# Kernel optimization log

Measured on AMD Instinct MI355X. Metric: run time of the kernel, lower is better.

The kernel has to match this reference:

```python
import jax, jax.numpy as jnp
import numpy as np

DIM = 1024
NUM_HEADS = 16
HEAD_DIM = DIM // NUM_HEADS
SCALE = float(np.sqrt(HEAD_DIM))
NEG = -1e9


def setup_inputs() -> dict:
    key = jax.random.key(0)
    ks = jax.random.split(key, 12)
    B, S = 2, 2048
    std = 1.0 / np.sqrt(DIM)
    inp = {
        'query': jax.random.normal(ks[0], (B, S, DIM), jnp.float32),
        'key': jax.random.normal(ks[1], (B, S, DIM), jnp.float32),
        'value': jax.random.normal(ks[2], (B, S, DIM), jnp.float32),
        'key_padding_mask': jnp.ones((B, S), jnp.int32),
        'Wq': jax.random.normal(ks[3], (DIM, DIM), jnp.float32) * std,
        'bq': jax.random.normal(ks[4], (DIM,), jnp.float32) * std,
        'Wk': jax.random.normal(ks[5], (DIM, DIM), jnp.float32) * std,
        'bk': jax.random.normal(ks[6], (DIM,), jnp.float32) * std,
        'Wv': jax.random.normal(ks[7], (DIM, DIM), jnp.float32) * std,
        'bv': jax.random.normal(ks[8], (DIM,), jnp.float32) * std,
        'Wo': jax.random.normal(ks[9], (DIM, DIM), jnp.float32) * std,
        'bo': jax.random.normal(ks[10], (DIM,), jnp.float32) * std,
    }
    return inp


def reference(query, key, value, key_padding_mask, Wq, bq, Wk, bk, Wv, bv, Wo, bo):
    B, S, _ = query.shape
    # QKV projections (torch Linear: x @ W.T + b), split heads -> [B,H,S,D]
    def proj(x, W, b):
        return (x @ W.T + b).reshape(B, -1, NUM_HEADS, HEAD_DIM).transpose(0, 2, 1, 3)
    Q = proj(query, Wq, bq)
    K = proj(key, Wk, bk)
    V = proj(value, Wv, bv)
    # scaled dot-product scores [B,H,Sq,Sk]
    scores = jnp.einsum('bhqd,bhkd->bhqk', Q, K) / SCALE
    # key padding mask: positions where mask == 0 are filled with -1e9
    pad = (key_padding_mask == 0)[:, None, None, :]  # [B,1,1,Sk]
    scores = jnp.where(pad, NEG, scores)
    attention_weights = jax.nn.softmax(scores, axis=-1)
    context = jnp.einsum('bhqk,bhkd->bhqd', attention_weights, V)
    context = context.transpose(0, 2, 1, 3).reshape(B, -1, DIM)
    out = context @ Wo.T + bo
    return out, attention_weights
```

## Files before the change

### kernel.cpp

```cpp
#include <hip/hip_runtime.h>
#include <hip/hip_bf16.h>
#include <stdint.h>

#define DIMM 1024
#define HEADS 16
#define HD 64
#define BB 2
#define SS 2048
#define NTOK (BB*SS)

typedef __attribute__((ext_vector_type(8))) __bf16 bf16x8;
typedef __attribute__((ext_vector_type(4))) __bf16 bf16x4;
typedef __attribute__((ext_vector_type(4))) float f32x4;

__device__ __forceinline__ f32x4 mfma16(bf16x8 a, bf16x8 b, f32x4 c) {
  return __builtin_amdgcn_mfma_f32_16x16x32_bf16(a, b, c, 0, 0, 0);
}

__device__ __forceinline__ void gload_lds16(const void* g, void* l) {
  __builtin_amdgcn_global_load_lds(
      (__attribute__((address_space(1))) void*)(void*)g,
      (__attribute__((address_space(3))) void*)l,
      16, 0, 0);
}

#define LOG2E 1.4426950408889634f
#define C2 (0.125f * LOG2E)
#define NBRAW (-8e9f)

struct CvtArgs {
  const float* src[7];
  __bf16* dst[7];
  int n[7];
};

__global__ __launch_bounds__(256) void cvt_kernel(CvtArgs a) {
  const int t = blockIdx.y;
  const long i = ((long)blockIdx.x * 256 + threadIdx.x) * 8;
  if (i >= a.n[t]) return;
  const float* s = a.src[t] + i;
  f32x4 x0 = *(const f32x4*)s;
  f32x4 x1 = *(const f32x4*)(s + 4);
  bf16x8 o;
  o[0] = (__bf16)x0[0]; o[1] = (__bf16)x0[1]; o[2] = (__bf16)x0[2]; o[3] = (__bf16)x0[3];
  o[4] = (__bf16)x1[0]; o[5] = (__bf16)x1[1]; o[6] = (__bf16)x1[2]; o[7] = (__bf16)x1[3];
  *(bf16x8*)(a.dst[t] + i) = o;
}

__global__ void maskbits_kernel(const int* __restrict__ msk, uint32_t* __restrict__ mbits) {
  int j = threadIdx.x;
  if (j >= 128) return;
  const int* src = msk + j * 32;
  uint32_t wdd = 0;
#pragma unroll
  for (int i = 0; i < 32; ++i) wdd |= (src[i] != 0 ? 1u : 0u) << i;
  mbits[j] = wdd;
}

struct GemmArgs {
  const __bf16* A[3];
  const __bf16* B[3];
  const float* bias[3];
  void* out[3];
  int mode[3];
};

__global__ __launch_bounds__(256) void gemm_bt(GemmArgs ga) {
  const int z = blockIdx.z;
  const __bf16* __restrict__ A  = ga.A[z];
  const __bf16* __restrict__ Bm = ga.B[z];
  const float* __restrict__ bias = ga.bias[z];
  void* Cout = ga.out[z];
  const int mode = ga.mode[z];

  __shared__ __align__(16) char sA[2][16384];
  __shared__ __align__(16) char sB[2][16384];
  const int tid = threadIdx.x;
  const int w = tid >> 6, l = tid & 63;
  const int wr = w >> 1, wc = w & 1;
  const int lg = l >> 4, lr = l & 15;
  const int m0 = blockIdx.y * 128, n0 = blockIdx.x * 128;

  f32x4 acc[4][4] = {};

  auto stage = [&](int k0, int buf) {
#pragma unroll
    for (int i = 0; i < 4; ++i) {
      int c = (i * 4 + w) * 64 + l;
      int row = c >> 3, ch = c & 7;
      gload_lds16(A + (size_t)(m0 + row) * 1024 + k0 + ((ch ^ (row & 7)) << 3),
                  &sA[buf][(i * 4 + w) * 1024]);
    }
#pragma unroll
    for (int i = 0; i < 4; ++i) {
      int c = (i * 4 + w) * 64 + l;
      int row = c >> 3, ch = c & 7;
      gload_lds16(Bm + (size_t)(n0 + row) * 1024 + k0 + ((ch ^ (row & 7)) << 3),
                  &sB[buf][(i * 4 + w) * 1024]);
    }
  };

  stage(0, 0);
  __syncthreads();

  for (int ks = 0; ks < 16; ++ks) {
    const int cur = ks & 1;
    if (ks < 15) stage((ks + 1) * 64, cur ^ 1);
#pragma unroll
    for (int kk = 0; kk < 2; ++kk) {
      bf16x8 af[4], bfv[4];
#pragma unroll
      for (int fm = 0; fm < 4; ++fm) {
        int row = wr * 64 + fm * 16 + lr;
        af[fm] = *(const bf16x8*)&sA[cur][row * 128 + (((kk * 4 + lg) ^ (row & 7)) << 4)];
      }
#pragma unroll
      for (int fn = 0; fn < 4; ++fn) {
        int row = wc * 64 + fn * 16 + lr;
        bfv[fn] = *(const bf16x8*)&sB[cur][row * 128 + (((kk * 4 + lg) ^ (row & 7)) << 4)];
      }
#pragma unroll
      for (int fm = 0; fm < 4; ++fm)
#pragma unroll
        for (int fn = 0; fn < 4; ++fn)
          acc[fm][fn] = mfma16(af[fm], bfv[fn], acc[fm][fn]);
    }
    __syncthreads();
  }

#pragma unroll
  for (int fm = 0; fm < 4; ++fm) {
#pragma unroll
    for (int fn = 0; fn < 4; ++fn) {
      const int n = n0 + wc * 64 + fn * 16 + lr;
      const int mb = m0 + wr * 64 + fm * 16 + 4 * lg;
      const float bval = bias[n];
      f32x4 vv = acc[fm][fn];
      if (mode == 2) {
        float* C = (float*)Cout;
#pragma unroll
        for (int r = 0; r < 4; ++r)
          C[(size_t)(mb + r) * 1024 + n] = vv[r] + bval;
      } else if (mode == 0) {
        __bf16* C = (__bf16*)Cout;
        const int hh = n >> 6, d = n & 63;
#pragma unroll
        for (int r = 0; r < 4; ++r) {
          int m = mb + r;
          C[(((size_t)(m >> 11) * 16 + hh) * 2048 + (m & 2047)) * 64 + d] =
              (__bf16)(vv[r] + bval);
        }
      } else {
        __bf16* C = (__bf16*)Cout;
        const int hh = n >> 6, d = n & 63;
        bf16x4 pk;
#pragma unroll
        for (int r = 0; r < 4; ++r) pk[r] = (__bf16)(vv[r] + bval);
        *(bf16x4*)(C + (((size_t)(mb >> 11) * 16 + hh) * 64 + d) * 2048 + (mb & 2047)) = pk;
      }
    }
  }
}

__global__ __launch_bounds__(256) void attn_kernel(
    const __bf16* __restrict__ Qh, const __bf16* __restrict__ Kh,
    const __bf16* __restrict__ Vt, const uint32_t* __restrict__ mbits,
    float* __restrict__ attnW, __bf16* __restrict__ ctx)
{
  __shared__ __align__(16) char sK[2][8192];
  __shared__ __align__(16) char sV[2][8192];
  __shared__ __align__(16) float sPF[4][16][32];

  const int tid = threadIdx.x;
  const int w = tid >> 6, l = tid & 63;
  const int lg = l >> 4, lr = l & 15;

  const int bid = blockIdx.x;
  const int xcd = bid & 7, j = bid >> 3;
  const int bh = xcd * 4 + (j >> 5);
  const int q0 = (j & 31) * 64;
  const int b = bh >> 4, h = bh & 15;

  const __bf16* qbase = Qh + ((size_t)bh * SS + q0 + w * 16 + lr) * HD;
  bf16x8 qf0 = *(const bf16x8*)(qbase + lg * 8);
  bf16x8 qf1 = *(const bf16x8*)(qbase + 32 + lg * 8);

  const __bf16* Khead = Kh + (size_t)bh * SS * HD;
  const __bf16* Vhead = Vt + (size_t)bh * HD * SS;
  const uint32_t* mrow = mbits + b * 64;

  const int c0 = w * 64 + l;

  auto stageK = [&](int k0, int buf) {
#pragma unroll
    for (int i = 0; i < 2; ++i) {
      int c = i * 256 + c0;
      int kr = c >> 3, ch = c & 7;
      gload_lds16(Khead + (size_t)(k0 + kr) * HD + ((ch ^ (kr & 7)) << 3),
                  &sK[buf][(i * 4 + w) * 1024]);
    }
  };
  auto stageV = [&](int k0, int buf) {
#pragma unroll
    for (int i = 0; i < 2; ++i) {
      int c = i * 256 + c0;
      int d = c >> 3, ch = c & 7;
      gload_lds16(Vhead + (size_t)d * SS + k0 + ((ch ^ (d & 7)) << 3),
                  &sV[buf][(i * 4 + w) * 1024]);
    }
  };

  stageK(0, 0);
  asm volatile("s_waitcnt vmcnt(0)" ::: "memory");
  __builtin_amdgcn_s_barrier();

  float lsum = 0.0f;

  for (int t = 0; t < 32; ++t) {
    const int cur = t & 1;
    if (t < 31) stageK((t + 1) * 64, cur ^ 1);

    const uint32_t mw0 = mrow[2 * t], mw1 = mrow[2 * t + 1];
    const bool fast = ((mw0 & mw1) == 0xFFFFFFFFu);

#pragma unroll
    for (int sub = 0; sub < 4; ++sub) {
      const int kr = sub * 16 + lr;
      bf16x8 k0f = *(const bf16x8*)&sK[cur][kr * 128 + ((lg ^ (kr & 7)) << 4)];
      bf16x8 k1f = *(const bf16x8*)&sK[cur][kr * 128 + (((4 + lg) ^ (kr & 7)) << 4)];
      __builtin_amdgcn_s_setprio(1);
      f32x4 a = {};
      a = mfma16(k0f, qf0, a);
      a = mfma16(k1f, qf1, a);
      __builtin_amdgcn_s_setprio(0);
      if (!fast) {
        uint32_t bits = ((sub < 2) ? mw0 : mw1) >> ((sub & 1) * 16 + 4 * lg);
#pragma unroll
        for (int r = 0; r < 4; ++r) a[r] = ((bits >> r) & 1) ? a[r] : NBRAW;
      }
#pragma unroll
      for (int r = 0; r < 4; ++r)
        lsum += __builtin_amdgcn_exp2f(fminf(a[r] * C2, 80.0f));
    }
    asm volatile("s_waitcnt vmcnt(0)" ::: "memory");
    __builtin_amdgcn_s_barrier();
  }

  lsum += __shfl_xor(lsum, 16);
  lsum += __shfl_xor(lsum, 32);
  const float rl = 1.0f / lsum;

  f32x4 Oa[4] = {};
  float* pwbase = attnW + ((size_t)bh * SS + q0 + w * 16) * SS;

  stageK(0, 0);
  stageV(0, 0);
  asm volatile("s_waitcnt vmcnt(0)" ::: "memory");
  __builtin_amdgcn_s_barrier();

  for (int t = 0; t < 32; ++t) {
    const int cur = t & 1;
    if (t < 31) { stageK((t + 1) * 64, cur ^ 1); stageV((t + 1) * 64, cur ^ 1); }

    const uint32_t mw0 = mrow[2 * t], mw1 = mrow[2 * t + 1];
    const bool fast = ((mw0 & mw1) == 0xFFFFFFFFu);

#pragma unroll
    for (int hh = 0; hh < 2; ++hh) {
#pragma unroll
      for (int s2 = 0; s2 < 2; ++s2) {
        const int sub = hh * 2 + s2;
        const int kr = sub * 16 + lr;
        bf16x8 k0f = *(const bf16x8*)&sK[cur][kr * 128 + ((lg ^ (kr & 7)) << 4)];
        bf16x8 k1f = *(const bf16x8*)&sK[cur][kr * 128 + (((4 + lg) ^ (kr & 7)) << 4)];
        __builtin_amdgcn_s_setprio(1);
        f32x4 a = {};
        a = mfma16(k0f, qf0, a);
        a = mfma16(k1f, qf1, a);
        __builtin_amdgcn_s_setprio(0);
        if (!fast) {
          uint32_t bits = ((sub < 2) ? mw0 : mw1) >> ((sub & 1) * 16 + 4 * lg);
#pragma unroll
          for (int r = 0; r < 4; ++r) a[r] = ((bits >> r) & 1) ? a[r] : NBRAW;
        }
        f32x4 p;
#pragma unroll
        for (int r = 0; r < 4; ++r)
          p[r] = __builtin_amdgcn_exp2f(fminf(a[r] * C2, 80.0f)) * rl;
        const int cp = (s2 * 4 + lg) ^ (lr & 7);
        *(f32x4*)&sPF[w][lr][cp * 4] = p;
      }

#pragma unroll
      for (int s2 = 0; s2 < 2; ++s2) {
        const int row = s2 * 8 + (l >> 3);
        const int cp = (l & 7) ^ (row & 7);
        f32x4 pv4 = *(const f32x4*)&sPF[w][row][cp * 4];
        __builtin_nontemporal_store(pv4,
            (f32x4*)(pwbase + (size_t)row * SS + t * 64 + hh * 32 + 4 * (l & 7)));
      }

      f32x4 pa_lo = *(const f32x4*)&sPF[w][lr][(((2 * lg) ^ (lr & 7)) * 4)];
      f32x4 pa_hi = *(const f32x4*)&sPF[w][lr][(((2 * lg + 1) ^ (lr & 7)) * 4)];
      bf16x8 pa;
#pragma unroll
      for (int r = 0; r < 4; ++r) {
        pa[r] = (__bf16)pa_lo[r];
        pa[4 + r] = (__bf16)pa_hi[r];
      }
      __builtin_amdgcn_s_setprio(1);
#pragma unroll
      for (int dg = 0; dg < 4; ++dg) {
        const int d = dg * 16 + lr;
        bf16x8 vb = *(const bf16x8*)&sV[cur][d * 128 + (((hh * 4 + lg) ^ (d & 7)) << 4)];
        Oa[dg] = mfma16(pa, vb, Oa[dg]);
      }
      __builtin_amdgcn_s_setprio(0);
    }

    asm volatile("s_waitcnt vmcnt(4)" ::: "memory");
    __builtin_amdgcn_s_barrier();
  }

#pragma unroll
  for (int dg = 0; dg < 4; ++dg)
#pragma unroll
    for (int r = 0; r < 4; ++r)
      ctx[(size_t)(b * SS + q0 + w * 16 + 4 * lg + r) * DIMM + h * HD + dg * 16 + lr] =
          (__bf16)Oa[dg][r];
}

extern "C" void kernel_launch(void* const* d_in, const int* in_sizes, int n_in,
                              void* d_out, int out_size, void* d_ws, size_t ws_size,
                              hipStream_t stream)
{
  const float* q   = (const float*)d_in[0];
  const float* k   = (const float*)d_in[1];
  const float* v   = (const float*)d_in[2];
  const int*   msk = (const int*)d_in[3];
  const float* Wq  = (const float*)d_in[4];
  const float* bq  = (const float*)d_in[5];
  const float* Wk  = (const float*)d_in[6];
  const float* bk  = (const float*)d_in[7];
  const float* Wv  = (const float*)d_in[8];
  const float* bv  = (const float*)d_in[9];
  const float* Wo  = (const float*)d_in[10];
  const float* bo  = (const float*)d_in[11];

  char* ws = (char*)d_ws;
  __bf16* xq  = (__bf16*)(ws);
  __bf16* xk  = (__bf16*)(ws + (8u << 20));
  __bf16* xv  = (__bf16*)(ws + (16u << 20));
  __bf16* wqb = (__bf16*)(ws + (24u << 20));
  __bf16* wkb = (__bf16*)(ws + (26u << 20));
  __bf16* wvb = (__bf16*)(ws + (28u << 20));
  __bf16* wob = (__bf16*)(ws + (30u << 20));
  __bf16* Qh  = (__bf16*)(ws + (32u << 20));
  __bf16* Kh  = (__bf16*)(ws + (40u << 20));
  __bf16* Vt  = (__bf16*)(ws + (48u << 20));
  __bf16* ctx = (__bf16*)(ws + (56u << 20));
  uint32_t* mbits = (uint32_t*)(ws + (64u << 20));

  CvtArgs ca;
  ca.src[0] = q;  ca.dst[0] = xq;  ca.n[0] = NTOK * DIMM;
  ca.src[1] = k;  ca.dst[1] = xk;  ca.n[1] = NTOK * DIMM;
  ca.src[2] = v;  ca.dst[2] = xv;  ca.n[2] = NTOK * DIMM;
  ca.src[3] = Wq; ca.dst[3] = wqb; ca.n[3] = DIMM * DIMM;
  ca.src[4] = Wk; ca.dst[4] = wkb; ca.n[4] = DIMM * DIMM;
  ca.src[5] = Wv; ca.dst[5] = wvb; ca.n[5] = DIMM * DIMM;
  ca.src[6] = Wo; ca.dst[6] = wob; ca.n[6] = DIMM * DIMM;
  cvt_kernel<<<dim3(2048, 7, 1), 256, 0, stream>>>(ca);
  maskbits_kernel<<<1, 128, 0, stream>>>(msk, mbits);

  GemmArgs g1;
  g1.A[0] = xq; g1.B[0] = wqb; g1.bias[0] = bq; g1.out[0] = (void*)Qh; g1.mode[0] = 0;
  g1.A[1] = xk; g1.B[1] = wkb; g1.bias[1] = bk; g1.out[1] = (void*)Kh; g1.mode[1] = 0;
  g1.A[2] = xv; g1.B[2] = wvb; g1.bias[2] = bv; g1.out[2] = (void*)Vt; g1.mode[2] = 1;
  gemm_bt<<<dim3(8, 32, 3), 256, 0, stream>>>(g1);

  float* out = (float*)d_out;
  float* attnW = out + (size_t)NTOK * DIMM;
  attn_kernel<<<dim3(1024, 1, 1), 256, 0, stream>>>(Qh, Kh, Vt, mbits, attnW, ctx);

  GemmArgs g2;
  g2.A[0] = ctx; g2.B[0] = wob; g2.bias[0] = bo; g2.out[0] = (void*)out; g2.mode[0] = 2;
  g2.A[1] = ctx; g2.B[1] = wob; g2.bias[1] = bo; g2.out[1] = (void*)out; g2.mode[1] = 2;
  g2.A[2] = ctx; g2.B[2] = wob; g2.bias[2] = bo; g2.out[2] = (void*)out; g2.mode[2] = 2;
  gemm_bt<<<dim3(8, 32, 1), 256, 0, stream>>>(g2);
}
```

Measured before the change: 248.4 us.

## Switch attention K/V staging to 32-key tiles with triple buffering

Halves the key tile per iteration from 64 to 32 and moves from double to triple buffering, so loads are prefetched two tiles ahead. The vmcnt waits are relaxed so the barrier only waits for the next tile, not the one just issued. The V layout swizzle changes to four chunks per row to match the narrower tile. The aim is to hide global load latency and cut LDS use, at the cost of twice as many loop iterations and barriers.

```diff
diff --git a/kernel.cpp b/kernel.cpp
--- a/kernel.cpp
+++ b/kernel.cpp
@@ -167,8 +167,8 @@
     const __bf16* __restrict__ Vt, const uint32_t* __restrict__ mbits,
     float* __restrict__ attnW, __bf16* __restrict__ ctx)
 {
-  __shared__ __align__(16) char sK[2][8192];
-  __shared__ __align__(16) char sV[2][8192];
+  __shared__ __align__(16) char sK[3][4096];
+  __shared__ __align__(16) char sV[3][4096];
   __shared__ __align__(16) float sPF[4][16][32];
 
   const int tid = threadIdx.x;
@@ -192,39 +192,32 @@
   const int c0 = w * 64 + l;
 
   auto stageK = [&](int k0, int buf) {
-#pragma unroll
-    for (int i = 0; i < 2; ++i) {
-      int c = i * 256 + c0;
-      int kr = c >> 3, ch = c & 7;
-      gload_lds16(Khead + (size_t)(k0 + kr) * HD + ((ch ^ (kr & 7)) << 3),
-                  &sK[buf][(i * 4 + w) * 1024]);
-    }
+    int kr = c0 >> 3, ch = c0 & 7;
+    gload_lds16(Khead + (size_t)(k0 + kr) * HD + ((ch ^ (kr & 7)) << 3),
+                &sK[buf][w * 1024]);
   };
   auto stageV = [&](int k0, int buf) {
-#pragma unroll
-    for (int i = 0; i < 2; ++i) {
-      int c = i * 256 + c0;
-      int d = c >> 3, ch = c & 7;
-      gload_lds16(Vhead + (size_t)d * SS + k0 + ((ch ^ (d & 7)) << 3),
-                  &sV[buf][(i * 4 + w) * 1024]);
-    }
+    int d = c0 >> 2, cs = c0 & 3;
+    gload_lds16(Vhead + (size_t)d * SS + k0 + ((cs ^ (d & 3)) << 3),
+                &sV[buf][w * 1024]);
   };
 
   stageK(0, 0);
-  asm volatile("s_waitcnt vmcnt(0)" ::: "memory");
+  stageK(32, 1);
+  asm volatile("s_waitcnt vmcnt(1)" ::: "memory");
   __builtin_amdgcn_s_barrier();
 
   float lsum = 0.0f;
 
-  for (int t = 0; t < 32; ++t) {
-    const int cur = t & 1;
-    if (t < 31) stageK((t + 1) * 64, cur ^ 1);
-
-    const uint32_t mw0 = mrow[2 * t], mw1 = mrow[2 * t + 1];
-    const bool fast = ((mw0 & mw1) == 0xFFFFFFFFu);
-
-#pragma unroll
-    for (int sub = 0; sub < 4; ++sub) {
+  for (int t = 0; t < 64; ++t) {
+    const int cur = t % 3;
+    if (t < 62) stageK((t + 2) * 32, (t + 2) % 3);
+
+    const uint32_t mw = mrow[t];
+    const bool fast = (mw == 0xFFFFFFFFu);
+
+#pragma unroll
+    for (int sub = 0; sub < 2; ++sub) {
       const int kr = sub * 16 + lr;
       bf16x8 k0f = *(const bf16x8*)&sK[cur][kr * 128 + ((lg ^ (kr & 7)) << 4)];
       bf16x8 k1f = *(const bf16x8*)&sK[cur][kr * 128 + (((4 + lg) ^ (kr & 7)) << 4)];
@@ -234,7 +227,7 @@
       a = mfma16(k1f, qf1, a);
       __builtin_amdgcn_s_setprio(0);
       if (!fast) {
-        uint32_t bits = ((sub < 2) ? mw0 : mw1) >> ((sub & 1) * 16 + 4 * lg);
+        uint32_t bits = mw >> (sub * 16 + 4 * lg);
 #pragma unroll
         for (int r = 0; r < 4; ++r) a[r] = ((bits >> r) & 1) ? a[r] : NBRAW;
       }
@@ -242,7 +235,7 @@
       for (int r = 0; r < 4; ++r)
         lsum += __builtin_amdgcn_exp2f(fminf(a[r] * C2, 80.0f));
     }
-    asm volatile("s_waitcnt vmcnt(0)" ::: "memory");
+    asm volatile("s_waitcnt vmcnt(1)" ::: "memory");
     __builtin_amdgcn_s_barrier();
   }
 
@@ -253,72 +246,68 @@
   f32x4 Oa[4] = {};
   float* pwbase = attnW + ((size_t)bh * SS + q0 + w * 16) * SS;
 
-  stageK(0, 0);
-  stageV(0, 0);
-  asm volatile("s_waitcnt vmcnt(0)" ::: "memory");
+  stageK(0, 0); stageV(0, 0);
+  stageK(32, 1); stageV(32, 1);
+  asm volatile("s_waitcnt vmcnt(2)" ::: "memory");
   __builtin_amdgcn_s_barrier();
 
-  for (int t = 0; t < 32; ++t) {
-    const int cur = t & 1;
-    if (t < 31) { stageK((t + 1) * 64, cur ^ 1); stageV((t + 1) * 64, cur ^ 1); }
-
-    const uint32_t mw0 = mrow[2 * t], mw1 = mrow[2 * t + 1];
-    const bool fast = ((mw0 & mw1) == 0xFFFFFFFFu);
-
-#pragma unroll
-    for (int hh = 0; hh < 2; ++hh) {
-#pragma unroll
-      for (int s2 = 0; s2 < 2; ++s2) {
-        const int sub = hh * 2 + s2;
-        const int kr = sub * 16 + lr;
-        bf16x8 k0f = *(const bf16x8*)&sK[cur][kr * 128 + ((lg ^ (kr & 7)) << 4)];
-        bf16x8 k1f = *(const bf16x8*)&sK[cur][kr * 128 + (((4 + lg) ^ (kr & 7)) << 4)];
-        __builtin_amdgcn_s_setprio(1);
-        f32x4 a = {};
-        a = mfma16(k0f, qf0, a);
-        a = mfma16(k1f, qf1, a);
-        __builtin_amdgcn_s_setprio(0);
-        if (!fast) {
-          uint32_t bits = ((sub < 2) ? mw0 : mw1) >> ((sub & 1) * 16 + 4 * lg);
-#pragma unroll
-          for (int r = 0; r < 4; ++r) a[r] = ((bits >> r) & 1) ? a[r] : NBRAW;
-        }
-        f32x4 p;
-#pragma unroll
-        for (int r = 0; r < 4; ++r)
-          p[r] = __builtin_amdgcn_exp2f(fminf(a[r] * C2, 80.0f)) * rl;
-        const int cp = (s2 * 4 + lg) ^ (lr & 7);
-        *(f32x4*)&sPF[w][lr][cp * 4] = p;
-      }
-
-#pragma unroll
-      for (int s2 = 0; s2 < 2; ++s2) {
-        const int row = s2 * 8 + (l >> 3);
-        const int cp = (l & 7) ^ (row & 7);
-        f32x4 pv4 = *(const f32x4*)&sPF[w][row][cp * 4];
-        __builtin_nontemporal_store(pv4,
-            (f32x4*)(pwbase + (size_t)row * SS + t * 64 + hh * 32 + 4 * (l & 7)));
-      }
-
-      f32x4 pa_lo = *(const f32x4*)&sPF[w][lr][(((2 * lg) ^ (lr & 7)) * 4)];
-      f32x4 pa_hi = *(const f32x4*)&sPF[w][lr][(((2 * lg + 1) ^ (lr & 7)) * 4)];
-      bf16x8 pa;
-#pragma unroll
-      for (int r = 0; r < 4; ++r) {
-        pa[r] = (__bf16)pa_lo[r];
-        pa[4 + r] = (__bf16)pa_hi[r];
-      }
+  for (int t = 0; t < 64; ++t) {
+    const int cur = t % 3;
+    if (t < 62) { stageK((t + 2) * 32, (t + 2) % 3); stageV((t + 2) * 32, (t + 2) % 3); }
+
+    const uint32_t mw = mrow[t];
+    const bool fast = (mw == 0xFFFFFFFFu);
+
+#pragma unroll
+    for (int sub = 0; sub < 2; ++sub) {
+      const int kr = sub * 16 + lr;
+      bf16x8 k0f = *(const bf16x8*)&sK[cur][kr * 128 + ((lg ^ (kr & 7)) << 4)];
+      bf16x8 k1f = *(const bf16x8*)&sK[cur][kr * 128 + (((4 + lg) ^ (kr & 7)) << 4)];
       __builtin_amdgcn_s_setprio(1);
-#pragma unroll
-      for (int dg = 0; dg < 4; ++dg) {
-        const int d = dg * 16 + lr;
-        bf16x8 vb = *(const bf16x8*)&sV[cur][d * 128 + (((hh * 4 + lg) ^ (d & 7)) << 4)];
-        Oa[dg] = mfma16(pa, vb, Oa[dg]);
-      }
+      f32x4 a = {};
+      a = mfma16(k0f, qf0, a);
+      a = mfma16(k1f, qf1, a);
       __builtin_amdgcn_s_setprio(0);
-    }
-
-    asm volatile("s_waitcnt vmcnt(4)" ::: "memory");
+      if (!fast) {
+        uint32_t bits = mw >> (sub * 16 + 4 * lg);
+#pragma unroll
+        for (int r = 0; r < 4; ++r) a[r] = ((bits >> r) & 1) ? a[r] : NBRAW;
+      }
+      f32x4 p;
+#pragma unroll
+      for (int r = 0; r < 4; ++r)
+        p[r] = __builtin_amdgcn_exp2f(fminf(a[r] * C2, 80.0f)) * rl;
+      const int cp = (sub * 4 + lg) ^ (lr & 7);
+      *(f32x4*)&sPF[w][lr][cp * 4] = p;
+    }
+
+#pragma unroll
+    for (int s2 = 0; s2 < 2; ++s2) {
+      const int row = s2 * 8 + (l >> 3);
+      const int cp = (l & 7) ^ (row & 7);
+      f32x4 pv4 = *(const f32x4*)&sPF[w][row][cp * 4];
+      __builtin_nontemporal_store(pv4,
+          (f32x4*)(pwbase + (size_t)row * SS + t * 32 + 4 * (l & 7)));
+    }
+
+    f32x4 pa_lo = *(const f32x4*)&sPF[w][lr][(((2 * lg) ^ (lr & 7)) * 4)];
+    f32x4 pa_hi = *(const f32x4*)&sPF[w][lr][(((2 * lg + 1) ^ (lr & 7)) * 4)];
+    bf16x8 pa;
+#pragma unroll
+    for (int r = 0; r < 4; ++r) {
+      pa[r] = (__bf16)pa_lo[r];
+      pa[4 + r] = (__bf16)pa_hi[r];
+    }
+    __builtin_amdgcn_s_setprio(1);
+#pragma unroll
+    for (int dg = 0; dg < 4; ++dg) {
+      const int d = dg * 16 + lr;
+      bf16x8 vb = *(const bf16x8*)&sV[cur][d * 64 + ((lg ^ (d & 3)) << 4)];
+      Oa[dg] = mfma16(pa, vb, Oa[dg]);
+    }
+    __builtin_amdgcn_s_setprio(0);
+
+    asm volatile("s_waitcnt vmcnt(6)" ::: "memory");
     __builtin_amdgcn_s_barrier();
   }
 
```

Result: slower. 258.6 us (+4.1%).
